# Kernel tuning notes

Hardware: AMD Instinct MI355X
Metric: run time of the kernel (lower is better)

The kernel has to match this reference:

```python
import jax, jax.numpy as jnp
import numpy as np
import math

D_MODEL = 1024
NUM_HEADS = 16
HEAD = D_MODEL // NUM_HEADS
EPS = 1e-5


def setup_inputs() -> dict:
    key = jax.random.key(0)
    ks = jax.random.split(key, 5)
    x = jax.random.normal(ks[0], (2, 2048, D_MODEL), dtype=jnp.float32)
    # parameters (torch.rand -> uniform [0,1) per the module; scaled here for numerics)
    wq = jax.random.uniform(ks[1], (NUM_HEADS, D_MODEL, HEAD), dtype=jnp.float32) * 0.02
    wk = jax.random.uniform(ks[2], (NUM_HEADS, D_MODEL, HEAD), dtype=jnp.float32) * 0.02
    wv = jax.random.uniform(ks[3], (NUM_HEADS, D_MODEL, HEAD), dtype=jnp.float32) * 0.02
    wo = jax.random.uniform(ks[4], (D_MODEL, D_MODEL), dtype=jnp.float32) * 0.02
    ln_w = jnp.ones((D_MODEL,), dtype=jnp.float32)
    ln_b = jnp.zeros((D_MODEL,), dtype=jnp.float32)
    return {"x": x, "ln_w": ln_w, "ln_b": ln_b, "wq": wq, "wk": wk, "wv": wv, "wo": wo}


def _layernorm(x, w, b):
    mean = jnp.mean(x, axis=-1, keepdims=True)
    var = jnp.var(x, axis=-1, keepdims=True)
    return (x - mean) * w / jnp.sqrt(var + EPS) + b


def reference(x, ln_w, ln_b, wq, wk, wv, wo):
    # pre-norm
    y = _layernorm(x, ln_w, ln_b)  # [b, s, d]
    seq_len = y.shape[-2]
    # per-head projections: [b, h, s, e]
    q = jnp.einsum('bsd,hde->bhse', y, wq)
    k = jnp.einsum('bsd,hde->bhse', y, wk)
    v = jnp.einsum('bsd,hde->bhse', y, wv)
    scores = jnp.einsum('bhse,bhte->bhst', q, k) / math.sqrt(HEAD)
    causal = jnp.triu(jnp.full((seq_len, seq_len), -jnp.inf, dtype=scores.dtype), k=1)
    scores = scores + causal
    weights = jax.nn.softmax(scores, axis=-1)
    attn = jnp.einsum('bhst,bhte->bshe', weights, v)  # merged transpose
    attn = attn.reshape(*attn.shape[:-2], -1)  # [b, s, d]
    out = attn @ wo
    return out + x
```

## Files before the change

kernel.cpp:

```cpp
#include <hip/hip_runtime.h>
#include <stdint.h>

typedef __bf16 bf16;
typedef __bf16 bf16x2 __attribute__((ext_vector_type(2)));
typedef __bf16 bf16x4 __attribute__((ext_vector_type(4)));
typedef __bf16 bf16x8 __attribute__((ext_vector_type(8)));
typedef float f32x4 __attribute__((ext_vector_type(4)));

#define D_MODEL 1024
#define NHEADS 16
#define HEADDIM 64
#define SEQ 2048
#define NBATCH 2

__device__ __forceinline__ void async_load16(const void* g, void* l) {
  __builtin_amdgcn_global_load_lds(
      (__attribute__((address_space(1))) void*)g,
      (__attribute__((address_space(3))) void*)l, 16, 0, 0);
}

__device__ __forceinline__ float fexp2(float x) {
#if __has_builtin(__builtin_amdgcn_exp2f)
  return __builtin_amdgcn_exp2f(x);
#else
  return exp2f(x);
#endif
}

__global__ __launch_bounds__(256)
void ln_and_transpose(const float* __restrict__ x, const float* __restrict__ lw,
                      const float* __restrict__ lb, bf16* __restrict__ y,
                      const float* __restrict__ wq, const float* __restrict__ wk,
                      const float* __restrict__ wv, const float* __restrict__ wo,
                      bf16* __restrict__ WqkvT, bf16* __restrict__ woT) {
  __shared__ float tile[64][65];
  __shared__ float ps[4], pq[4];
  int t = threadIdx.x;
  if (blockIdx.x < 4096) {
    int row = blockIdx.x;
    const float4 v = ((const float4*)(x + (size_t)row * D_MODEL))[t];
    float s = v.x + v.y + v.z + v.w;
    float sq = v.x * v.x + v.y * v.y + v.z * v.z + v.w * v.w;
#pragma unroll
    for (int d = 1; d < 64; d <<= 1) {
      s += __shfl_xor(s, d);
      sq += __shfl_xor(sq, d);
    }
    if ((t & 63) == 0) { ps[t >> 6] = s; pq[t >> 6] = sq; }
    __syncthreads();
    s = ps[0] + ps[1] + ps[2] + ps[3];
    sq = pq[0] + pq[1] + pq[2] + pq[3];
    float mean = s * (1.0f / D_MODEL);
    float var = sq * (1.0f / D_MODEL) - mean * mean;
    float rstd = rsqrtf(var + 1e-5f);
    float4 wv4 = ((const float4*)lw)[t];
    float4 bv = ((const float4*)lb)[t];
    bf16x4 o;
    o[0] = (bf16)((v.x - mean) * rstd * wv4.x + bv.x);
    o[1] = (bf16)((v.y - mean) * rstd * wv4.y + bv.y);
    o[2] = (bf16)((v.z - mean) * rstd * wv4.z + bv.z);
    o[3] = (bf16)((v.w - mean) * rstd * wv4.w + bv.w);
    ((bf16x4*)(y + (size_t)row * D_MODEL))[t] = o;
    return;
  }
  int blk = blockIdx.x - 4096;
  const float* s;
  bf16* d;
  int src_ld, dst_ld;
  if (blk < 768) {
    int wsel = blk >> 8;
    int rem = blk & 255;
    int h = rem >> 4, tr = rem & 15;
    const float* w3 = (wsel == 0) ? wq : (wsel == 1) ? wk : wv;
    s = w3 + (size_t)h * 65536 + (size_t)tr * 64 * 64;
    d = WqkvT + ((size_t)wsel << 20) + (size_t)h * 65536 + (size_t)tr * 64;
    src_ld = 64; dst_ld = 1024;
  } else {
    int r = blk - 768;
    int tr = r >> 4, tc = r & 15;
    s = wo + (size_t)(tr * 64) * 1024 + tc * 64;
    d = woT + (size_t)(tc * 64) * 1024 + tr * 64;
    src_ld = 1024; dst_ld = 1024;
  }
  int rr = t >> 4;
  int cc = (t & 15) << 2;
#pragma unroll
  for (int i = 0; i < 4; ++i) {
    float4 v = *(const float4*)&s[(size_t)(rr + i * 16) * src_ld + cc];
    tile[rr + i * 16][cc + 0] = v.x;
    tile[rr + i * 16][cc + 1] = v.y;
    tile[rr + i * 16][cc + 2] = v.z;
    tile[rr + i * 16][cc + 3] = v.w;
  }
  __syncthreads();
#pragma unroll
  for (int i = 0; i < 4; ++i) {
    int drow = rr + i * 16;
    bf16x4 o;
    o[0] = (bf16)tile[cc + 0][drow];
    o[1] = (bf16)tile[cc + 1][drow];
    o[2] = (bf16)tile[cc + 2][drow];
    o[3] = (bf16)tile[cc + 3][drow];
    *(bf16x4*)&d[(size_t)drow * dst_ld + cc] = o;
  }
}

template <int MODE, int BM, int BN>
__global__ __launch_bounds__(256)
void gemm_bt(const bf16* __restrict__ A, const bf16* __restrict__ Bt,
             int ntn, void* __restrict__ p0, void* __restrict__ p1,
             void* __restrict__ p2) {
  constexpr int NWR = BM / 64;
  constexpr int NWC = 4 / NWR;
  constexpr int NJ = BN / (16 * NWC);
  __shared__ __align__(16) bf16 As[2][BM * 64];
  __shared__ __align__(16) bf16 Bs[2][BN * 64];
  int cpx = gridDim.x >> 3;
  int wg = (blockIdx.x & 7) * cpx + (blockIdx.x >> 3);
  int bm = wg / ntn;
  int bn = wg % ntn;
  int t = threadIdx.x;
  int w = t >> 6, l = t & 63;
  int lg = l >> 4, lo = l & 15;
  int wr = w / NWC, wc = w % NWC;
  const bf16* Ab = A + (size_t)bm * BM * 1024;
  const bf16* Bb = Bt + (size_t)bn * BN * 1024;
  f32x4 acc[4][NJ];
#pragma unroll
  for (int i = 0; i < 4; ++i)
#pragma unroll
    for (int j = 0; j < NJ; ++j) acc[i][j] = (f32x4){0.f, 0.f, 0.f, 0.f};

  auto stage = [&](int bufi, int k0) {
#pragma unroll
    for (int it = 0; it < BM / 32; ++it) {
      int flat = it * 2048 + t * 8;
      int row = flat >> 6, sc = ((flat & 63) >> 3) ^ (row & 7);
      async_load16(Ab + (size_t)row * 1024 + k0 + sc * 8, &As[bufi][it * 2048 + w * 512]);
    }
#pragma unroll
    for (int it = 0; it < BN / 32; ++it) {
      int flat = it * 2048 + t * 8;
      int row = flat >> 6, sc = ((flat & 63) >> 3) ^ (row & 7);
      async_load16(Bb + (size_t)row * 1024 + k0 + sc * 8, &Bs[bufi][it * 2048 + w * 512]);
    }
  };

  stage(0, 0);
  __syncthreads();
  int buf = 0;
  for (int k0 = 0; k0 < 1024; k0 += 64) {
    if (k0 + 64 < 1024) stage(buf ^ 1, k0 + 64);
#pragma unroll
    for (int kk = 0; kk < 2; ++kk) {
      bf16x8 af[4], bfr[NJ];
#pragma unroll
      for (int i = 0; i < 4; ++i) {
        int row = wr * 64 + i * 16 + lo;
        af[i] = *(const bf16x8*)&As[buf][row * 64 + (((4 * kk + lg) ^ (lo & 7)) * 8)];
      }
#pragma unroll
      for (int j = 0; j < NJ; ++j) {
        int row = wc * (NJ * 16) + j * 16 + lo;
        bfr[j] = *(const bf16x8*)&Bs[buf][row * 64 + (((4 * kk + lg) ^ (lo & 7)) * 8)];
      }
#pragma unroll
      for (int i = 0; i < 4; ++i)
#pragma unroll
        for (int j = 0; j < NJ; ++j)
          acc[i][j] = __builtin_amdgcn_mfma_f32_16x16x32_bf16(af[i], bfr[j], acc[i][j], 0, 0, 0);
    }
    __syncthreads();
    buf ^= 1;
  }

  int mbase = bm * BM + wr * 64;
  int nbase = bn * BN + wc * (NJ * 16);
#pragma unroll
  for (int i = 0; i < 4; ++i) {
#pragma unroll
    for (int j = 0; j < NJ; ++j) {
      int row0 = mbase + i * 16 + lg * 4;
      int col = nbase + j * 16 + lo;
      if (MODE == 0) {
        if (col < 2048) {
          bf16* dst = (bf16*)(col < 1024 ? p0 : p1);
          int c = col & 1023;
          int h = c >> 6, e = c & 63;
#pragma unroll
          for (int r = 0; r < 4; ++r) {
            int row = row0 + r;
            dst[((((size_t)(row >> 11) * NHEADS + h) * SEQ) + (row & 2047)) * HEADDIM + e] =
                (bf16)acc[i][j][r];
          }
        } else {
          int c = col - 2048;
          int h = c >> 6, e = c & 63;
          int b_ = row0 >> 11, s_ = row0 & 2047;
          bf16x4 pk;
          pk[0] = (bf16)acc[i][j][0]; pk[1] = (bf16)acc[i][j][1];
          pk[2] = (bf16)acc[i][j][2]; pk[3] = (bf16)acc[i][j][3];
          *(bf16x4*)&((bf16*)p2)[(((size_t)b_ * NHEADS + h) * HEADDIM + e) * SEQ + s_] = pk;
        }
      } else {
#pragma unroll
        for (int r = 0; r < 4; ++r) {
          int row = row0 + r;
          float xr = ((const float*)p1)[(size_t)row * 1024 + col];
          ((float*)p0)[(size_t)row * 1024 + col] = acc[i][j][r] + xr;
        }
      }
    }
  }
}

__global__ __launch_bounds__(512)
void attn_kernel(const bf16* __restrict__ q, const bf16* __restrict__ k,
                 const bf16* __restrict__ vt, bf16* __restrict__ attn) {
  __shared__ __align__(16) bf16 Ks[2][64 * 64];
  __shared__ __align__(16) bf16 Vs[2][64 * 64];
  __shared__ __align__(16) bf16 P[8][16 * 64];
  const float C2 = 0.125f * 1.44269504f;
  const float MC = 128.0f * C2;
  int i = blockIdx.x;
  int slot = i >> 3;
  int bh = (i & 7) + 8 * (slot >> 4);
  int tb = (slot & 32) ? (slot & 15) : 15 - (slot & 15);
  int b = bh >> 4, h = bh & 15;
  int t = threadIdx.x, w = t >> 6, l = t & 63;
  int lg = l >> 4, lo = l & 15;
  const bf16* qp = q + (size_t)bh * SEQ * HEADDIM;
  const bf16* kp = k + (size_t)bh * SEQ * HEADDIM;
  const bf16* vp = vt + (size_t)bh * HEADDIM * SEQ;
  int q0 = tb * 128 + w * 16;
  int cd = q0 >> 6;
  int nc = 2 * tb + 2;

  bf16x8 qf0 = *(const bf16x8*)&qp[(size_t)(q0 + lo) * HEADDIM + 8 * lg];
  bf16x8 qf1 = *(const bf16x8*)&qp[(size_t)(q0 + lo) * HEADDIM + 32 + 8 * lg];

  auto stage = [&](int bufi, int kv0) {
    int row = t >> 3, c16 = t & 7;
    int sc = c16 ^ (row & 7);
    async_load16(kp + (size_t)(kv0 + row) * HEADDIM + sc * 8, &Ks[bufi][(t >> 6) * 512 + (t & 63) * 8]);
    async_load16(vp + (size_t)row * SEQ + kv0 + sc * 8, &Vs[bufi][(t >> 6) * 512 + (t & 63) * 8]);
  };

  f32x4 o[4];
#pragma unroll
  for (int nt = 0; nt < 4; ++nt) o[nt] = (f32x4){0.f, 0.f, 0.f, 0.f};
  float lsum = 0.f;
  int diag_rhs = (w & 3) * 16 + lo;

  int buf = 0;
  stage(0, 0);
  __syncthreads();

  for (int c = 0; c < nc; ++c) {
    if (c + 1 < nc) stage(buf ^ 1, (c + 1) * 64);

    if (c <= cd) {
      f32x4 s[4];
      __builtin_amdgcn_s_setprio(1);
#pragma unroll
      for (int nt = 0; nt < 4; ++nt) {
        s[nt] = (f32x4){0.f, 0.f, 0.f, 0.f};
        int krow = nt * 16 + lo;
        bf16x8 kf0 = *(const bf16x8*)&Ks[buf][krow * 64 + ((lg ^ (lo & 7)) * 8)];
        bf16x8 kf1 = *(const bf16x8*)&Ks[buf][krow * 64 + (((4 + lg) ^ (lo & 7)) * 8)];
        s[nt] = __builtin_amdgcn_mfma_f32_16x16x32_bf16(kf0, qf0, s[nt], 0, 0, 0);
        s[nt] = __builtin_amdgcn_mfma_f32_16x16x32_bf16(kf1, qf1, s[nt], 0, 0, 0);
      }
      __builtin_amdgcn_s_setprio(0);

      bf16x8 vf0[4], vf1[4];
#pragma unroll
      for (int nt = 0; nt < 4; ++nt) {
        int vrow = nt * 16 + lo;
        vf0[nt] = *(const bf16x8*)&Vs[buf][vrow * 64 + ((lg ^ (lo & 7)) * 8)];
        vf1[nt] = *(const bf16x8*)&Vs[buf][vrow * 64 + (((4 + lg) ^ (lo & 7)) * 8)];
      }

      if (c == cd) {
#pragma unroll
        for (int nt = 0; nt < 4; ++nt)
#pragma unroll
          for (int r = 0; r < 4; ++r)
            s[nt][r] = (16 * nt + 4 * lg + r <= diag_rhs) ? s[nt][r] : -1e30f;
      }

      float p[4][4];
      float psum[4];
#pragma unroll
      for (int nt = 0; nt < 4; ++nt) {
        psum[nt] = 0.f;
#pragma unroll
        for (int r = 0; r < 4; ++r) {
          float e = fexp2(fmaf(s[nt][r], C2, -MC));
          p[nt][r] = e;
          psum[nt] += e;
        }
      }
      float pst = (psum[0] + psum[1]) + (psum[2] + psum[3]);
      pst += __shfl_xor(pst, 16);
      pst += __shfl_xor(pst, 32);
      lsum += pst;

#pragma unroll
      for (int nt = 0; nt < 4; ++nt) {
        int chunk = (2 * nt + (lg >> 1)) ^ (lo & 7);
        int base = lo * 64 + chunk * 8 + 4 * (lg & 1);
        bf16x2 w0, w1;
        w0[0] = (bf16)p[nt][0]; w0[1] = (bf16)p[nt][1];
        w1[0] = (bf16)p[nt][2]; w1[1] = (bf16)p[nt][3];
        *(bf16x2*)&P[w][base] = w0;
        *(bf16x2*)&P[w][base + 2] = w1;
      }
      bf16x8 pf0 = *(const bf16x8*)&P[w][lo * 64 + ((lg ^ (lo & 7)) * 8)];
      bf16x8 pf1 = *(const bf16x8*)&P[w][lo * 64 + (((4 + lg) ^ (lo & 7)) * 8)];

      __builtin_amdgcn_s_setprio(1);
#pragma unroll
      for (int nt = 0; nt < 4; ++nt) {
        o[nt] = __builtin_amdgcn_mfma_f32_16x16x32_bf16(pf0, vf0[nt], o[nt], 0, 0, 0);
        o[nt] = __builtin_amdgcn_mfma_f32_16x16x32_bf16(pf1, vf1[nt], o[nt], 0, 0, 0);
      }
      __builtin_amdgcn_s_setprio(0);
    }

    __syncthreads();
    buf ^= 1;
  }

#pragma unroll
  for (int r = 0; r < 4; ++r) {
    float ls = __shfl(lsum, (l & 48) | (4 * lg + r));
    float inv = 1.0f / ls;
    int qrow = q0 + 4 * lg + r;
#pragma unroll
    for (int nt = 0; nt < 4; ++nt)
      attn[((size_t)b * SEQ + qrow) * D_MODEL + h * HEADDIM + nt * 16 + lo] =
          (bf16)(o[nt][r] * inv);
  }
}

extern "C" void kernel_launch(void* const* d_in, const int* in_sizes, int n_in,
                              void* d_out, int out_size, void* d_ws, size_t ws_size,
                              hipStream_t stream) {
  const float* x = (const float*)d_in[0];
  const float* ln_w = (const float*)d_in[1];
  const float* ln_b = (const float*)d_in[2];
  const float* wq = (const float*)d_in[3];
  const float* wk = (const float*)d_in[4];
  const float* wv = (const float*)d_in[5];
  const float* wo = (const float*)d_in[6];
  float* out = (float*)d_out;
  char* ws = (char*)d_ws;

  bf16* y     = (bf16*)(ws);
  bf16* WqkvT = (bf16*)(ws + (8u << 20));
  bf16* woT   = (bf16*)(ws + (14u << 20));
  bf16* qb    = (bf16*)(ws + (16u << 20));
  bf16* kb    = (bf16*)(ws + (24u << 20));
  bf16* vtb   = (bf16*)(ws + (32u << 20));
  bf16* attnb = (bf16*)(ws + (40u << 20));

  ln_and_transpose<<<5120, 256, 0, stream>>>(x, ln_w, ln_b, y, wq, wk, wv, wo,
                                             WqkvT, woT);

  gemm_bt<0, 128, 192><<<512, 256, 0, stream>>>(y, WqkvT, 16, qb, kb, vtb);

  attn_kernel<<<dim3(512), 512, 0, stream>>>(qb, kb, vtb, attnb);

  gemm_bt<2, 64, 128><<<512, 256, 0, stream>>>(attnb, woT, 8, out, (void*)x, nullptr);
}
```

Baseline: 99.94 us.

## Split long causal attention query tiles across two blocks and merge partials

Measured after the change: 99.88 us. No clear change (-0.1%).

```diff
diff --git a/kernel.cpp b/kernel.cpp
--- a/kernel.cpp
+++ b/kernel.cpp
@@ -216,7 +216,8 @@
 
 __global__ __launch_bounds__(512)
 void attn_kernel(const bf16* __restrict__ q, const bf16* __restrict__ k,
-                 const bf16* __restrict__ vt, bf16* __restrict__ attn) {
+                 const bf16* __restrict__ vt, bf16* __restrict__ attn,
+                 bf16* __restrict__ pO, float* __restrict__ plsum) {
   __shared__ __align__(16) bf16 Ks[2][64 * 64];
   __shared__ __align__(16) bf16 Vs[2][64 * 64];
   __shared__ __align__(16) bf16 P[8][16 * 64];
@@ -224,8 +225,13 @@
   const float MC = 128.0f * C2;
   int i = blockIdx.x;
   int slot = i >> 3;
-  int bh = (i & 7) + 8 * (slot >> 4);
-  int tb = (slot & 32) ? (slot & 15) : 15 - (slot & 15);
+  int bh = (i & 7) + 8 * (slot & 3);
+  int ji = slot >> 2;
+  int split, tb;
+  if (ji < 8) { split = 0; tb = ji; }
+  else { split = 1 + ((ji >> 4) & 1); tb = 15 - (ji & 7); }
+  int c0 = (split == 2) ? tb + 1 : 0;
+  int c1 = (split == 1) ? tb + 1 : 2 * tb + 2;
   int b = bh >> 4, h = bh & 15;
   int t = threadIdx.x, w = t >> 6, l = t & 63;
   int lg = l >> 4, lo = l & 15;
@@ -234,7 +240,7 @@
   const bf16* vp = vt + (size_t)bh * HEADDIM * SEQ;
   int q0 = tb * 128 + w * 16;
   int cd = q0 >> 6;
-  int nc = 2 * tb + 2;
+  int diag_rhs = (w & 3) * 16 + lo;
 
   bf16x8 qf0 = *(const bf16x8*)&qp[(size_t)(q0 + lo) * HEADDIM + 8 * lg];
   bf16x8 qf1 = *(const bf16x8*)&qp[(size_t)(q0 + lo) * HEADDIM + 32 + 8 * lg];
@@ -250,14 +256,13 @@
 #pragma unroll
   for (int nt = 0; nt < 4; ++nt) o[nt] = (f32x4){0.f, 0.f, 0.f, 0.f};
   float lsum = 0.f;
-  int diag_rhs = (w & 3) * 16 + lo;
 
   int buf = 0;
-  stage(0, 0);
+  stage(0, c0 * 64);
   __syncthreads();
 
-  for (int c = 0; c < nc; ++c) {
-    if (c + 1 < nc) stage(buf ^ 1, (c + 1) * 64);
+  for (int c = c0; c < c1; ++c) {
+    if (c + 1 < c1) stage(buf ^ 1, (c + 1) * 64);
 
     if (c <= cd) {
       f32x4 s[4];
@@ -332,16 +337,50 @@
     buf ^= 1;
   }
 
-#pragma unroll
-  for (int r = 0; r < 4; ++r) {
-    float ls = __shfl(lsum, (l & 48) | (4 * lg + r));
-    float inv = 1.0f / ls;
-    int qrow = q0 + 4 * lg + r;
-#pragma unroll
-    for (int nt = 0; nt < 4; ++nt)
-      attn[((size_t)b * SEQ + qrow) * D_MODEL + h * HEADDIM + nt * 16 + lo] =
-          (bf16)(o[nt][r] * inv);
-  }
+  if (split == 0) {
+#pragma unroll
+    for (int r = 0; r < 4; ++r) {
+      float ls = __shfl(lsum, (l & 48) | (4 * lg + r));
+      float inv = 1.0f / ls;
+      int qrow = q0 + 4 * lg + r;
+#pragma unroll
+      for (int nt = 0; nt < 4; ++nt)
+        attn[((size_t)b * SEQ + qrow) * D_MODEL + h * HEADDIM + nt * 16 + lo] =
+            (bf16)(o[nt][r] * inv);
+    }
+  } else {
+    int half = split - 1;
+#pragma unroll
+    for (int r = 0; r < 4; ++r) {
+      float ls = __shfl(lsum, (l & 48) | (4 * lg + r));
+      int prow = q0 - 1024 + 4 * lg + r;
+      if (lo == 0) plsum[(half << 15) + (bh << 10) + prow] = ls;
+      size_t base = (((size_t)half * 32 + bh) * 1024 + prow) * 64;
+#pragma unroll
+      for (int nt = 0; nt < 4; ++nt)
+        pO[base + nt * 16 + lo] = (bf16)o[nt][r];
+    }
+  }
+}
+
+__global__ __launch_bounds__(256)
+void merge_kernel(const bf16* __restrict__ pO, const float* __restrict__ plsum,
+                  bf16* __restrict__ attn) {
+  int tid = blockIdx.x * 256 + threadIdx.x;
+  int bh = tid >> 14;
+  int rem = tid & 16383;
+  int srow = rem >> 4, q4 = rem & 15;
+  int b = bh >> 4, h = bh & 15;
+  float l = plsum[(bh << 10) + srow] + plsum[(1 << 15) + (bh << 10) + srow];
+  float inv = 1.0f / l;
+  size_t base = (((size_t)bh) * 1024 + srow) * 64 + q4 * 4;
+  bf16x4 a1 = *(const bf16x4*)&pO[base];
+  bf16x4 a2 = *(const bf16x4*)&pO[(size_t)32 * 1024 * 64 + base];
+  bf16x4 o;
+#pragma unroll
+  for (int e = 0; e < 4; ++e)
+    o[e] = (bf16)(((float)a1[e] + (float)a2[e]) * inv);
+  *(bf16x4*)&attn[((size_t)b * SEQ + 1024 + srow) * D_MODEL + h * HEADDIM + q4 * 4] = o;
 }
 
 extern "C" void kernel_launch(void* const* d_in, const int* in_sizes, int n_in,
@@ -364,13 +403,17 @@
   bf16* kb    = (bf16*)(ws + (24u << 20));
   bf16* vtb   = (bf16*)(ws + (32u << 20));
   bf16* attnb = (bf16*)(ws + (40u << 20));
+  bf16*  pO    = (bf16*)(ws);
+  float* plsum = (float*)(ws + (8u << 20));
 
   ln_and_transpose<<<5120, 256, 0, stream>>>(x, ln_w, ln_b, y, wq, wk, wv, wo,
                                              WqkvT, woT);
 
   gemm_bt<0, 128, 192><<<512, 256, 0, stream>>>(y, WqkvT, 16, qb, kb, vtb);
 
-  attn_kernel<<<dim3(512), 512, 0, stream>>>(qb, kb, vtb, attnb);
+  attn_kernel<<<dim3(768), 512, 0, stream>>>(qb, kb, vtb, attnb, pO, plsum);
+
+  merge_kernel<<<2048, 256, 0, stream>>>(pO, plsum, attnb);
 
   gemm_bt<2, 64, 128><<<512, 256, 0, stream>>>(attnb, woT, 8, out, (void*)x, nullptr);
 }
```
